# Performance work log

Hardware: AMD Instinct MI355X
Metric: run time of the kernel (lower is better)

## Reference

```python
import jax, jax.numpy as jnp
import numpy as np

N = 4194304          # total nodes
NUM_GRAPHS = 8192    # segments
T_STEPS = 1000       # num_diffusion_timestep
S = 1e-4             # noise precision
POWER = 3.0


def polynomial_alpha_schedule():
    # Faithful to E3DiffusionProcess.polynomial_schedule + clip_noise_schedule.
    x = jnp.linspace(0.0, T_STEPS, T_STEPS + 1)
    alphas2 = (1.0 - (x / T_STEPS) ** POWER) ** 2
    alphas2 = jnp.concatenate([jnp.ones((1,), alphas2.dtype), alphas2])
    step = jnp.clip(alphas2[1:] / alphas2[:-1], 0.001, 1.0)
    alphas2 = jnp.cumprod(step)
    return (1.0 - 2.0 * S) * alphas2 + S  # this IS self.alpha_schedule in the module


def segment_mean_remove(x, batch_index):
    # remove_mean with batch_index: subtract per-graph mean, single pass.
    sums = jax.ops.segment_sum(x, batch_index, num_segments=NUM_GRAPHS)
    cnts = jax.ops.segment_sum(jnp.ones((x.shape[0], 1), x.dtype), batch_index,
                               num_segments=NUM_GRAPHS)
    mean = sums / jnp.maximum(cnts, 1.0)
    return x - mean[batch_index]


def setup_inputs() -> dict:
    key = jax.random.key(0)
    k1, k2 = jax.random.split(key)
    z = jax.random.normal(k1, (N, 3), dtype=jnp.float32)
    noise = jax.random.normal(k2, (N, 3), dtype=jnp.float32)
    batch_index = jnp.sort(jax.random.randint(jax.random.key(1), (N,), 0, NUM_GRAPHS))
    return {"z": z, "noise": noise, "batch_index": batch_index, "t": 500}


def reference(z, noise, batch_index, t):
    # diffuse_zero_to_t with mode='pos', segmented remove_mean over graphs.
    alpha_sched = polynomial_alpha_schedule()
    alpha_t = alpha_sched[t]
    sigma_t = jnp.sqrt(1.0 - alpha_t ** 2)
    noise_c = segment_mean_remove(noise, batch_index)
    z_after = alpha_t * z + sigma_t * noise_c
    return (z_after, noise_c)
```

## Files before the change

### kernel.cpp

```cpp
#include <hip/hip_runtime.h>
#include <math.h>

#define NN 4194304
#define NG 8192
#define TSTEPS 1000


__global__ __launch_bounds__(256) void k_alpha(const int* __restrict__ t_ptr,
                                               float* __restrict__ wsf) {
    int t = t_ptr[0];
    int tid = threadIdx.x;
    double partial = 1.0;
    #pragma unroll
    for (int k = 0; k < 4; ++k) {
        int j = tid * 4 + k;
        if (j <= TSTEPS && j <= t) {
            double xj = (double)j / (double)TSTEPS;
            double num = 1.0 - xj * xj * xj; num *= num;
            double den = 1.0;
            if (j > 0) {
                double xp = (double)(j - 1) / (double)TSTEPS;
                den = 1.0 - xp * xp * xp; den *= den;
            }
            double step = num / den;
            step = fmin(fmax(step, 0.001), 1.0);
            partial *= step;
        }
    }
    #pragma unroll
    for (int off = 1; off < 64; off <<= 1)
        partial *= __shfl_xor(partial, off);
    __shared__ double wprod[4];
    int lane = tid & 63, wid = tid >> 6;
    if (lane == 0) wprod[wid] = partial;
    __syncthreads();
    if (tid == 0) {
        double P = wprod[0] * wprod[1] * wprod[2] * wprod[3];
        double at = (1.0 - 2.0e-4) * P + 1.0e-4;
        wsf[0] = (float)at;
        wsf[1] = (float)sqrt(1.0 - at * at);
    }
}

__global__ void k_bounds(const int* __restrict__ bidx, int* __restrict__ start, int n) {
    int i = blockIdx.x * blockDim.x + threadIdx.x;
    if (i >= n) return;
    int b = bidx[i];
    if (i == 0) {
        for (int s = 0; s <= b; ++s) start[s] = 0;
    } else {
        int pb = bidx[i - 1];
        for (int s = pb + 1; s <= b; ++s) start[s] = i;
    }
    if (i == n - 1) {
        for (int s = b + 1; s <= NG; ++s) start[s] = n;
    }
}

__global__ __launch_bounds__(256) void k_segmean(const float* __restrict__ noise,
                                                 const int* __restrict__ start,
                                                 float4* __restrict__ mean) {
    int s = blockIdx.x;
    int rs = start[s], re = start[s + 1];
    int cnt = re - rs;
    float sx = 0.f, sy = 0.f, sz = 0.f;
    for (int i = rs + (int)threadIdx.x; i < re; i += 256) {
        sx += noise[3 * i + 0];
        sy += noise[3 * i + 1];
        sz += noise[3 * i + 2];
    }
    #pragma unroll
    for (int off = 32; off > 0; off >>= 1) {
        sx += __shfl_down(sx, off);
        sy += __shfl_down(sy, off);
        sz += __shfl_down(sz, off);
    }
    __shared__ float red[3][4];
    int lane = threadIdx.x & 63, wid = threadIdx.x >> 6;
    if (lane == 0) { red[0][wid] = sx; red[1][wid] = sy; red[2][wid] = sz; }
    __syncthreads();
    if (threadIdx.x == 0) {
        float inv = 1.0f / (float)(cnt > 1 ? cnt : 1);
        float mx = (red[0][0] + red[0][1] + red[0][2] + red[0][3]) * inv;
        float my = (red[1][0] + red[1][1] + red[1][2] + red[1][3]) * inv;
        float mz = (red[2][0] + red[2][1] + red[2][2] + red[2][3]) * inv;
        mean[s] = make_float4(mx, my, mz, 0.f);
    }
}

__global__ __launch_bounds__(256) void k_main(const float* __restrict__ z,
                                              const float* __restrict__ noise,
                                              const int* __restrict__ bidx,
                                              const float* __restrict__ wsf,
                                              const float4* __restrict__ mean,
                                              float* __restrict__ out) {
    int g = blockIdx.x * blockDim.x + threadIdx.x;
    float alpha = wsf[0], sigma = wsf[1];
    const float4* zp = (const float4*)z + (size_t)g * 3;
    const float4* np = (const float4*)noise + (size_t)g * 3;
    float4 z0 = zp[0], z1 = zp[1], z2 = zp[2];
    float4 n0 = np[0], n1 = np[1], n2 = np[2];
    int4 b = ((const int4*)bidx)[g];
    float4 m0 = mean[b.x], m1 = mean[b.y], m2 = mean[b.z], m3 = mean[b.w];

    float4 c0, c1, c2;
    c0.x = n0.x - m0.x; c0.y = n0.y - m0.y; c0.z = n0.z - m0.z; c0.w = n0.w - m1.x;
    c1.x = n1.x - m1.y; c1.y = n1.y - m1.z; c1.z = n1.z - m2.x; c1.w = n1.w - m2.y;
    c2.x = n2.x - m2.z; c2.y = n2.y - m3.x; c2.z = n2.z - m3.y; c2.w = n2.w - m3.z;

    float4 a0, a1, a2;
    a0.x = alpha * z0.x + sigma * c0.x; a0.y = alpha * z0.y + sigma * c0.y;
    a0.z = alpha * z0.z + sigma * c0.z; a0.w = alpha * z0.w + sigma * c0.w;
    a1.x = alpha * z1.x + sigma * c1.x; a1.y = alpha * z1.y + sigma * c1.y;
    a1.z = alpha * z1.z + sigma * c1.z; a1.w = alpha * z1.w + sigma * c1.w;
    a2.x = alpha * z2.x + sigma * c2.x; a2.y = alpha * z2.y + sigma * c2.y;
    a2.z = alpha * z2.z + sigma * c2.z; a2.w = alpha * z2.w + sigma * c2.w;

    float4* oz = (float4*)out + (size_t)g * 3;
    float4* oc = (float4*)(out + (size_t)NN * 3) + (size_t)g * 3;
    oz[0] = a0; oz[1] = a1; oz[2] = a2;
    oc[0] = c0; oc[1] = c1; oc[2] = c2;
}

extern "C" void kernel_launch(void* const* d_in, const int* in_sizes, int n_in,
                              void* d_out, int out_size, void* d_ws, size_t ws_size,
                              hipStream_t stream) {
    const float* z     = (const float*)d_in[0];
    const float* noise = (const float*)d_in[1];
    const int*   bidx  = (const int*)d_in[2];
    const int*   t     = (const int*)d_in[3];
    float* out = (float*)d_out;

    float*  wsf   = (float*)d_ws;
    int*    start = (int*)(wsf + 4);
    float4* mean  = (float4*)(wsf + 8200);

    k_alpha<<<1, 256, 0, stream>>>(t, wsf);
    k_bounds<<<NN / 256, 256, 0, stream>>>(bidx, start, NN);
    k_segmean<<<NG, 256, 0, stream>>>(noise, start, mean);
    k_main<<<NN / 4 / 256, 256, 0, stream>>>(z, noise, bidx, wsf, mean, out);
}
```

Before: 213.3 us.

## Fuse segment mean and apply into one per-segment kernel

Merges the segment-mean kernel and the elementwise apply kernel into a single per-segment block kernel. Each block computes its segment's mean, then re-reads noise (likely from cache) and z to write both outputs. This removes one launch, the mean buffer, and the batch_index reread in the main pass. The trade-off is scalar strided 3-float loads and stores in place of float4 vectorised access, and occupancy that depends on segment-sized blocks.

```diff
diff --git a/kernel.cpp b/kernel.cpp
--- a/kernel.cpp
+++ b/kernel.cpp
@@ -57,14 +57,18 @@
     }
 }
 
-__global__ __launch_bounds__(256) void k_segmean(const float* __restrict__ noise,
-                                                 const int* __restrict__ start,
-                                                 float4* __restrict__ mean) {
+__global__ __launch_bounds__(256) void k_fused(const float* __restrict__ noise,
+                                               const float* __restrict__ z,
+                                               const int* __restrict__ start,
+                                               const float* __restrict__ wsf,
+                                               float* __restrict__ out) {
     int s = blockIdx.x;
     int rs = start[s], re = start[s + 1];
     int cnt = re - rs;
+    int tid = threadIdx.x;
+
     float sx = 0.f, sy = 0.f, sz = 0.f;
-    for (int i = rs + (int)threadIdx.x; i < re; i += 256) {
+    for (int i = rs + tid; i < re; i += 256) {
         sx += noise[3 * i + 0];
         sy += noise[3 * i + 1];
         sz += noise[3 * i + 2];
@@ -76,50 +80,35 @@
         sz += __shfl_down(sz, off);
     }
     __shared__ float red[3][4];
-    int lane = threadIdx.x & 63, wid = threadIdx.x >> 6;
+    __shared__ float m[3];
+    int lane = tid & 63, wid = tid >> 6;
     if (lane == 0) { red[0][wid] = sx; red[1][wid] = sy; red[2][wid] = sz; }
     __syncthreads();
-    if (threadIdx.x == 0) {
+    if (tid == 0) {
         float inv = 1.0f / (float)(cnt > 1 ? cnt : 1);
-        float mx = (red[0][0] + red[0][1] + red[0][2] + red[0][3]) * inv;
-        float my = (red[1][0] + red[1][1] + red[1][2] + red[1][3]) * inv;
-        float mz = (red[2][0] + red[2][1] + red[2][2] + red[2][3]) * inv;
-        mean[s] = make_float4(mx, my, mz, 0.f);
+        m[0] = (red[0][0] + red[0][1] + red[0][2] + red[0][3]) * inv;
+        m[1] = (red[1][0] + red[1][1] + red[1][2] + red[1][3]) * inv;
+        m[2] = (red[2][0] + red[2][1] + red[2][2] + red[2][3]) * inv;
     }
-}
+    __syncthreads();
+    float mx = m[0], my = m[1], mz = m[2];
+    float alpha = wsf[0], sigma = wsf[1];
 
-__global__ __launch_bounds__(256) void k_main(const float* __restrict__ z,
-                                              const float* __restrict__ noise,
-                                              const int* __restrict__ bidx,
-                                              const float* __restrict__ wsf,
-                                              const float4* __restrict__ mean,
-                                              float* __restrict__ out) {
-    int g = blockIdx.x * blockDim.x + threadIdx.x;
-    float alpha = wsf[0], sigma = wsf[1];
-    const float4* zp = (const float4*)z + (size_t)g * 3;
-    const float4* np = (const float4*)noise + (size_t)g * 3;
-    float4 z0 = zp[0], z1 = zp[1], z2 = zp[2];
-    float4 n0 = np[0], n1 = np[1], n2 = np[2];
-    int4 b = ((const int4*)bidx)[g];
-    float4 m0 = mean[b.x], m1 = mean[b.y], m2 = mean[b.z], m3 = mean[b.w];
-
-    float4 c0, c1, c2;
-    c0.x = n0.x - m0.x; c0.y = n0.y - m0.y; c0.z = n0.z - m0.z; c0.w = n0.w - m1.x;
-    c1.x = n1.x - m1.y; c1.y = n1.y - m1.z; c1.z = n1.z - m2.x; c1.w = n1.w - m2.y;
-    c2.x = n2.x - m2.z; c2.y = n2.y - m3.x; c2.z = n2.z - m3.y; c2.w = n2.w - m3.z;
-
-    float4 a0, a1, a2;
-    a0.x = alpha * z0.x + sigma * c0.x; a0.y = alpha * z0.y + sigma * c0.y;
-    a0.z = alpha * z0.z + sigma * c0.z; a0.w = alpha * z0.w + sigma * c0.w;
-    a1.x = alpha * z1.x + sigma * c1.x; a1.y = alpha * z1.y + sigma * c1.y;
-    a1.z = alpha * z1.z + sigma * c1.z; a1.w = alpha * z1.w + sigma * c1.w;
-    a2.x = alpha * z2.x + sigma * c2.x; a2.y = alpha * z2.y + sigma * c2.y;
-    a2.z = alpha * z2.z + sigma * c2.z; a2.w = alpha * z2.w + sigma * c2.w;
-
-    float4* oz = (float4*)out + (size_t)g * 3;
-    float4* oc = (float4*)(out + (size_t)NN * 3) + (size_t)g * 3;
-    oz[0] = a0; oz[1] = a1; oz[2] = a2;
-    oc[0] = c0; oc[1] = c1; oc[2] = c2;
+    float* __restrict__ oc = out + (size_t)NN * 3;
+    for (int i = rs + tid; i < re; i += 256) {
+        float cx = noise[3 * i + 0] - mx;
+        float cy = noise[3 * i + 1] - my;
+        float cz = noise[3 * i + 2] - mz;
+        float zx = z[3 * i + 0];
+        float zy = z[3 * i + 1];
+        float zz = z[3 * i + 2];
+        out[3 * i + 0] = alpha * zx + sigma * cx;
+        out[3 * i + 1] = alpha * zy + sigma * cy;
+        out[3 * i + 2] = alpha * zz + sigma * cz;
+        oc[3 * i + 0] = cx;
+        oc[3 * i + 1] = cy;
+        oc[3 * i + 2] = cz;
+    }
 }
 
 extern "C" void kernel_launch(void* const* d_in, const int* in_sizes, int n_in,
@@ -131,12 +120,10 @@
     const int*   t     = (const int*)d_in[3];
     float* out = (float*)d_out;
 
-    float*  wsf   = (float*)d_ws;
-    int*    start = (int*)(wsf + 4);
-    float4* mean  = (float4*)(wsf + 8200);
+    float* wsf   = (float*)d_ws;
+    int*   start = (int*)(wsf + 4);
 
     k_alpha<<<1, 256, 0, stream>>>(t, wsf);
     k_bounds<<<NN / 256, 256, 0, stream>>>(bidx, start, NN);
-    k_segmean<<<NG, 256, 0, stream>>>(noise, start, mean);
-    k_main<<<NN / 4 / 256, 256, 0, stream>>>(z, noise, bidx, wsf, mean, out);
+    k_fused<<<NG, 256, 0, stream>>>(noise, z, start, wsf, out);
 }
```

Result: faster. 203.1 us (-4.8%).
